# Performance work log

Hardware: AMD Instinct MI355X
Metric: run time of the kernel (lower is better)

## Reference

```python
import jax, jax.numpy as jnp
import numpy as np

D_K = 64  # head dim used for scaling, matches init d_k


def setup_inputs() -> dict:
    key = jax.random.key(0)
    k1, k2, k3 = jax.random.split(key, 3)
    shape = (2, 2048, 16, 64)  # [batch, seq, heads, head_dim]
    q = jax.random.normal(k1, shape, dtype=jnp.float32)
    k = jax.random.normal(k2, shape, dtype=jnp.float32)
    v = jax.random.normal(k3, shape, dtype=jnp.float32)
    return {"q": q, "k": k, "v": v}


def reference(q, k, v):
    # score: [n, h, q, k]
    scale = 1.0 / np.sqrt(D_K).astype(np.float32)
    score = jnp.einsum('nqhd,nkhd->nhqk', q, k) * scale
    attn = jax.nn.softmax(score, axis=-1)
    context = jnp.einsum('nhqk,nkhd->nqhd', attn, v)
    return (context, attn)
```

## Files before the change

kernel.cpp:

```cpp
#include <hip/hip_runtime.h>

#define BATCH 2
#define SEQ   2048
#define NH    16
#define HD    64
#define RS    (NH*HD)
#define NPAIR (BATCH*NH)
#define NKT   (SEQ/64)
#define TILE_SHORTS 4096

typedef float f32x4  __attribute__((ext_vector_type(4)));
typedef short short8 __attribute__((ext_vector_type(8)));

#define GAS __attribute__((address_space(1)))
#define LAS __attribute__((address_space(3)))

__device__ __forceinline__ unsigned f2bf(float f) {
    union { float f; unsigned u; } c; c.f = f;
    return (c.u + 0x7FFFu + ((c.u >> 16) & 1u)) >> 16;
}
__device__ __forceinline__ unsigned pk(float lo, float hi) {
    return f2bf(lo) | (f2bf(hi) << 16);
}
__device__ __forceinline__ int swz(int row, int bc) {
    return (row * 128 + bc) ^ ((row & 7) << 4);
}
__device__ __forceinline__ short8 ld16(const void* p) {
    union { uint4 u; short8 s; } cv;
    cv.u = *(const uint4*)p;
    return cv.s;
}

__device__ __forceinline__ void load_qfrag(const float* Qr, int ks, short8& bq0, short8& bq1) {
    union { unsigned u[4]; short8 s; } t;
    float4 f0 = *(const float4*)(Qr + ks * 8);
    float4 f1 = *(const float4*)(Qr + ks * 8 + 4);
    t.u[0] = pk(f0.x * 0.125f, f0.y * 0.125f);
    t.u[1] = pk(f0.z * 0.125f, f0.w * 0.125f);
    t.u[2] = pk(f1.x * 0.125f, f1.y * 0.125f);
    t.u[3] = pk(f1.z * 0.125f, f1.w * 0.125f);
    bq0 = t.s;
    float4 g0 = *(const float4*)(Qr + 32 + ks * 8);
    float4 g1 = *(const float4*)(Qr + 32 + ks * 8 + 4);
    t.u[0] = pk(g0.x * 0.125f, g0.y * 0.125f);
    t.u[1] = pk(g0.z * 0.125f, g0.w * 0.125f);
    t.u[2] = pk(g1.x * 0.125f, g1.y * 0.125f);
    t.u[3] = pk(g1.z * 0.125f, g1.w * 0.125f);
    bq1 = t.s;
}

__device__ __forceinline__ void stage_k_from_f32(const float* Kt, unsigned short* Ksh, int tid) {
    #pragma unroll
    for (int i = 0; i < 2; ++i) {
        int cidx = tid + i * 256;
        int c = cidx >> 7, j = (cidx >> 6) & 1, l = cidx & 63;
        const float* src = Kt + (c * 16 + (l & 15)) * RS + j * 32 + (l >> 4) * 8;
        float4 f0 = *(const float4*)src;
        float4 f1 = *(const float4*)(src + 4);
        uint4 o = { pk(f0.x, f0.y), pk(f0.z, f0.w), pk(f1.x, f1.y), pk(f1.z, f1.w) };
        *((uint4*)Ksh + cidx) = o;
    }
}

extern "C" __global__ __launch_bounds__(256)
void pack_kv(const float* __restrict__ k, const float* __restrict__ v,
             unsigned short* __restrict__ ktl, unsigned short* __restrict__ vtl)
{
    __shared__ float Vf[64 * 65];
    const int bid = blockIdx.x;
    const int tid = threadIdx.x;

    if (bid < NPAIR * NKT) {
        const int kti = bid & 31, h = (bid >> 5) & 15, n = bid >> 9;
        const float* Kg = k + (((long)n * SEQ + kti * 64) * NH + h) * HD;
        stage_k_from_f32(Kg, ktl + (long)bid * TILE_SHORTS, tid);
    } else {
        const int b2 = bid - NPAIR * NKT;
        const int kti = b2 & 31, h = (b2 >> 5) & 15, n = b2 >> 9;
        const float* Vg = v + (((long)n * SEQ + kti * 64) * NH + h) * HD;
        #pragma unroll
        for (int i = 0; i < 4; ++i) {
            int idx = tid + i * 256;
            int row = idx >> 4, c4 = idx & 15;
            float4 f = *(const float4*)(Vg + row * RS + c4 * 4);
            Vf[row * 65 + c4 * 4 + 0] = f.x;
            Vf[row * 65 + c4 * 4 + 1] = f.y;
            Vf[row * 65 + c4 * 4 + 2] = f.z;
            Vf[row * 65 + c4 * 4 + 3] = f.w;
        }
        __syncthreads();
        uint4* out = (uint4*)(vtl + (long)b2 * TILE_SHORTS);
        #pragma unroll
        for (int i = 0; i < 2; ++i) {
            int cidx = tid + i * 256;
            int c = cidx >> 7, j = (cidx >> 6) & 1, l = cidx & 63;
            int d = c * 16 + (l & 15);
            int kb = j * 32 + (l >> 4) * 8;
            float a0 = Vf[(kb + 0) * 65 + d], a1 = Vf[(kb + 1) * 65 + d];
            float a2 = Vf[(kb + 2) * 65 + d], a3 = Vf[(kb + 3) * 65 + d];
            float a4 = Vf[(kb + 4) * 65 + d], a5 = Vf[(kb + 5) * 65 + d];
            float a6 = Vf[(kb + 6) * 65 + d], a7 = Vf[(kb + 7) * 65 + d];
            uint4 o = { pk(a0, a1), pk(a2, a3), pk(a4, a5), pk(a6, a7) };
            out[cidx] = o;
        }
    }
}

extern "C" __global__ __launch_bounds__(256, 4)
void sdpa_kernel(const float* __restrict__ q,
                 const unsigned short* __restrict__ ktl,
                 const unsigned short* __restrict__ vtl,
                 float* __restrict__ ctx, float* __restrict__ attn,
                 float* __restrict__ linv_out, int skip_pair)
{
    __shared__ unsigned short Kd[2][TILE_SHORTS];
    __shared__ unsigned short Vd[2][TILE_SHORTS];
    __shared__ unsigned short Ps[4][1024];

    const int bid0 = blockIdx.x;
    const int bid  = ((bid0 & 7) << 7) | (bid0 >> 3);
    const int qt = bid & 31, pair = bid >> 5;
    const int h = pair & 15, n = pair >> 4;
    const int tid = threadIdx.x;
    const int w = tid >> 6, lane = tid & 63, lh = lane & 15, ks = lane >> 4;
    const bool wattn = (pair != skip_pair);

    const float* Qr = q + (((long)n * SEQ + qt * 64 + w * 16 + lh) * NH + h) * HD;
    short8 bq0, bq1;
    load_qfrag(Qr, ks, bq0, bq1);

    const unsigned short* Ktile = ktl + (long)pair * NKT * TILE_SHORTS;
    const unsigned short* Vtile = vtl + (long)pair * NKT * TILE_SHORTS;

    auto stage = [&](unsigned short* lbuf, const unsigned short* gt) {
        #pragma unroll
        for (int i = 0; i < 2; ++i) {
            const unsigned short* g = gt + w * 1024 + i * 512 + lane * 8;
            unsigned short* l = lbuf + w * 1024 + i * 512;
            __builtin_amdgcn_global_load_lds((const GAS unsigned int*)g,
                                             (LAS unsigned int*)l, 16, 0, 0);
        }
    };

    stage(Kd[0], Ktile);
    asm volatile("s_waitcnt vmcnt(0)" ::: "memory");
    __builtin_amdgcn_s_barrier();
    float lsum = 0.f;
    for (int kt = 0; kt < NKT; ++kt) {
        const int cur = kt & 1;
        if (kt < NKT - 1) stage(Kd[cur ^ 1], Ktile + (kt + 1) * TILE_SHORTS);
        const char* Kb = (const char*)Kd[cur];
        #pragma unroll
        for (int c = 0; c < 4; ++c) {
            short8 a0 = ld16(Kb + ((c * 2 + 0) * 64 + lane) * 16);
            short8 a1 = ld16(Kb + ((c * 2 + 1) * 64 + lane) * 16);
            f32x4 z = {0.f, 0.f, 0.f, 0.f};
            z = __builtin_amdgcn_mfma_f32_16x16x32_bf16(a0, bq0, z, 0, 0, 0);
            z = __builtin_amdgcn_mfma_f32_16x16x32_bf16(a1, bq1, z, 0, 0, 0);
            lsum += __expf(z[0]) + __expf(z[1]) + __expf(z[2]) + __expf(z[3]);
        }
        asm volatile("s_waitcnt vmcnt(0)" ::: "memory");
        __builtin_amdgcn_s_barrier();
    }
    lsum += __shfl_xor(lsum, 16);
    lsum += __shfl_xor(lsum, 32);
    const float linv = 1.0f / lsum;

    if (pair == skip_pair && linv_out && ks == 0) {
        linv_out[qt * 64 + w * 16 + lh] = linv;
    }

    f32x4 oacc[4];
    #pragma unroll
    for (int cd = 0; cd < 4; ++cd) oacc[cd] = (f32x4){0.f, 0.f, 0.f, 0.f};

    float* attnW = attn + (((long)pair) * SEQ + qt * 64 + w * 16 + lh) * SEQ + ks * 4;
    char* Pw = (char*)Ps[w];

    stage(Kd[0], Ktile);
    stage(Vd[0], Vtile);
    asm volatile("s_waitcnt vmcnt(0)" ::: "memory");
    __builtin_amdgcn_s_barrier();

    for (int kt = 0; kt < NKT; ++kt) {
        const int cur = kt & 1;
        if (kt < NKT - 1) {
            stage(Kd[cur ^ 1], Ktile + (kt + 1) * TILE_SHORTS);
            stage(Vd[cur ^ 1], Vtile + (kt + 1) * TILE_SHORTS);
        }
        asm volatile("" ::: "memory");

        const char* Kb = (const char*)Kd[cur];
        f32x4 s[4];
        #pragma unroll
        for (int c = 0; c < 4; ++c) {
            short8 a0 = ld16(Kb + ((c * 2 + 0) * 64 + lane) * 16);
            short8 a1 = ld16(Kb + ((c * 2 + 1) * 64 + lane) * 16);
            f32x4 z = {0.f, 0.f, 0.f, 0.f};
            z = __builtin_amdgcn_mfma_f32_16x16x32_bf16(a0, bq0, z, 0, 0, 0);
            z = __builtin_amdgcn_mfma_f32_16x16x32_bf16(a1, bq1, z, 0, 0, 0);
            s[c] = z;
        }
        #pragma unroll
        for (int c = 0; c < 4; ++c) {
            f32x4 pv;
            pv[0] = __expf(s[c][0]) * linv;
            pv[1] = __expf(s[c][1]) * linv;
            pv[2] = __expf(s[c][2]) * linv;
            pv[3] = __expf(s[c][3]) * linv;
            if (wattn) {
                __builtin_nontemporal_store(pv, (f32x4*)(attnW + (long)kt * 64 + c * 16));
            }
            uint2 u2 = { pk(pv[0], pv[1]), pk(pv[2], pv[3]) };
            *(uint2*)(Pw + swz(lh, c * 32 + ks * 8)) = u2;
        }
        short8 pa0 = ld16(Pw + swz(lh, ks * 16));
        short8 pa1 = ld16(Pw + swz(lh, 64 + ks * 16));
        const char* Vb = (const char*)Vd[cur];
        #pragma unroll
        for (int cd = 0; cd < 4; ++cd) {
            short8 bv0 = ld16(Vb + ((cd * 2 + 0) * 64 + lane) * 16);
            short8 bv1 = ld16(Vb + ((cd * 2 + 1) * 64 + lane) * 16);
            oacc[cd] = __builtin_amdgcn_mfma_f32_16x16x32_bf16(pa0, bv0, oacc[cd], 0, 0, 0);
            oacc[cd] = __builtin_amdgcn_mfma_f32_16x16x32_bf16(pa1, bv1, oacc[cd], 0, 0, 0);
        }
        if (kt < NKT - 1) {
            if (wattn) asm volatile("s_waitcnt vmcnt(4)" ::: "memory");
            else       asm volatile("s_waitcnt vmcnt(0)" ::: "memory");
            __builtin_amdgcn_s_barrier();
        }
    }

    float* ctxW = ctx + (((long)n * SEQ + qt * 64 + w * 16 + ks * 4) * NH + h) * HD + lh;
    #pragma unroll
    for (int cd = 0; cd < 4; ++cd) {
        #pragma unroll
        for (int r = 0; r < 4; ++r) {
            ctxW[r * RS + cd * 16] = oacc[cd][r];
        }
    }
}

extern "C" __global__ __launch_bounds__(256)
void attn_fill_fast(const float* __restrict__ q, const float* __restrict__ k,
                    float* __restrict__ attn, const float* __restrict__ linv_in,
                    int pair)
{
    __shared__ unsigned short Ksh[TILE_SHORTS];
    const int n = pair >> 4, h = pair & 15;
    const int qt = blockIdx.x & 31, kt = blockIdx.x >> 5;
    const int tid = threadIdx.x;
    const int w = tid >> 6, lane = tid & 63, lh = lane & 15, ks = lane >> 4;

    const float* Qr = q + (((long)n * SEQ + qt * 64 + w * 16 + lh) * NH + h) * HD;
    short8 bq0, bq1;
    load_qfrag(Qr, ks, bq0, bq1);
    const float linv = linv_in[qt * 64 + w * 16 + lh];

    const float* Kt = k + (((long)n * SEQ + kt * 64) * NH + h) * HD;
    stage_k_from_f32(Kt, Ksh, tid);
    __syncthreads();

    float* attnW = attn + (((long)pair) * SEQ + qt * 64 + w * 16 + lh) * SEQ + ks * 4;
    #pragma unroll
    for (int c = 0; c < 4; ++c) {
        short8 a0 = ld16((const char*)Ksh + ((c * 2 + 0) * 64 + lane) * 16);
        short8 a1 = ld16((const char*)Ksh + ((c * 2 + 1) * 64 + lane) * 16);
        f32x4 z = {0.f, 0.f, 0.f, 0.f};
        z = __builtin_amdgcn_mfma_f32_16x16x32_bf16(a0, bq0, z, 0, 0, 0);
        z = __builtin_amdgcn_mfma_f32_16x16x32_bf16(a1, bq1, z, 0, 0, 0);
        f32x4 pv;
        pv[0] = __expf(z[0]) * linv;
        pv[1] = __expf(z[1]) * linv;
        pv[2] = __expf(z[2]) * linv;
        pv[3] = __expf(z[3]) * linv;
        __builtin_nontemporal_store(pv, (f32x4*)(attnW + (long)kt * 64 + c * 16));
    }
}

extern "C" __global__ __launch_bounds__(256, 4)
void attn_fill_slow(const float* __restrict__ q, const float* __restrict__ k,
                    float* __restrict__ attn, int pair)
{
    __shared__ unsigned short Ksh[TILE_SHORTS];
    const int n = pair >> 4, h = pair & 15;
    const int qt = blockIdx.x;
    const int tid = threadIdx.x;
    const int w = tid >> 6, lane = tid & 63, lh = lane & 15, ks = lane >> 4;

    const float* Qr = q + (((long)n * SEQ + qt * 64 + w * 16 + lh) * NH + h) * HD;
    short8 bq0, bq1;
    load_qfrag(Qr, ks, bq0, bq1);

    const float* Kg = k + ((long)n * SEQ * NH + h) * HD;

    float lsum = 0.f;
    for (int kt = 0; kt < NKT; ++kt) {
        __syncthreads();
        stage_k_from_f32(Kg + (long)kt * 64 * RS, Ksh, tid);
        __syncthreads();
        #pragma unroll
        for (int c = 0; c < 4; ++c) {
            short8 a0 = ld16((const char*)Ksh + ((c * 2 + 0) * 64 + lane) * 16);
            short8 a1 = ld16((const char*)Ksh + ((c * 2 + 1) * 64 + lane) * 16);
            f32x4 z = {0.f, 0.f, 0.f, 0.f};
            z = __builtin_amdgcn_mfma_f32_16x16x32_bf16(a0, bq0, z, 0, 0, 0);
            z = __builtin_amdgcn_mfma_f32_16x16x32_bf16(a1, bq1, z, 0, 0, 0);
            lsum += __expf(z[0]) + __expf(z[1]) + __expf(z[2]) + __expf(z[3]);
        }
    }
    lsum += __shfl_xor(lsum, 16);
    lsum += __shfl_xor(lsum, 32);
    const float linv = 1.0f / lsum;

    float* attnW = attn + (((long)pair) * SEQ + qt * 64 + w * 16 + lh) * SEQ + ks * 4;
    for (int kt = 0; kt < NKT; ++kt) {
        __syncthreads();
        stage_k_from_f32(Kg + (long)kt * 64 * RS, Ksh, tid);
        __syncthreads();
        #pragma unroll
        for (int c = 0; c < 4; ++c) {
            short8 a0 = ld16((const char*)Ksh + ((c * 2 + 0) * 64 + lane) * 16);
            short8 a1 = ld16((const char*)Ksh + ((c * 2 + 1) * 64 + lane) * 16);
            f32x4 z = {0.f, 0.f, 0.f, 0.f};
            z = __builtin_amdgcn_mfma_f32_16x16x32_bf16(a0, bq0, z, 0, 0, 0);
            z = __builtin_amdgcn_mfma_f32_16x16x32_bf16(a1, bq1, z, 0, 0, 0);
            f32x4 pv;
            pv[0] = __expf(z[0]) * linv;
            pv[1] = __expf(z[1]) * linv;
            pv[2] = __expf(z[2]) * linv;
            pv[3] = __expf(z[3]) * linv;
            *(f32x4*)(attnW + (long)kt * 64 + c * 16) = pv;
        }
    }
}

extern "C" void kernel_launch(void* const* d_in, const int* in_sizes, int n_in,
                              void* d_out, int out_size, void* d_ws, size_t ws_size,
                              hipStream_t stream)
{
    const float* q = (const float*)d_in[0];
    const float* k = (const float*)d_in[1];
    const float* v = (const float*)d_in[2];
    float* ctx  = (float*)d_out;
    float* attn = ctx + (size_t)BATCH * SEQ * NH * HD;

    const size_t tiles_shorts = (size_t)NPAIR * NKT * TILE_SHORTS;
    const size_t ws_need = 2 * tiles_shorts * sizeof(unsigned short);

    unsigned short *ktl, *vtl;
    int skip;
    if (ws_size >= ws_need) {
        ktl = (unsigned short*)d_ws;
        vtl = ktl + tiles_shorts;
        skip = -1;
    } else {
        ktl = (unsigned short*)(attn + (size_t)(NPAIR - 1) * SEQ * SEQ);
        vtl = ktl + tiles_shorts;
        skip = NPAIR - 1;
    }

    const bool linv_fits = (ws_size >= SEQ * sizeof(float));
    float* linv_ws = (skip >= 0 && linv_fits) ? (float*)d_ws : nullptr;

    hipLaunchKernelGGL(pack_kv, dim3(2 * NPAIR * NKT), dim3(256), 0, stream, k, v, ktl, vtl);
    hipLaunchKernelGGL(sdpa_kernel, dim3(NPAIR * NKT), dim3(256), 0, stream,
                       q, ktl, vtl, ctx, attn, linv_ws, skip);
    if (skip >= 0) {
        if (linv_ws) {
            hipLaunchKernelGGL(attn_fill_fast, dim3(NKT * 32), dim3(256), 0, stream,
                               q, k, attn, linv_ws, skip);
        } else {
            hipLaunchKernelGGL(attn_fill_slow, dim3(32), dim3(256), 0, stream, q, k, attn, skip);
        }
    }
}
```

Baseline: 208.6 us.

## Deepen K prefetch in row-sum pass and fold normalization into exp2

The first pass, which only computes softmax row sums, now prefetches K tiles two steps ahead through a four-buffer ring. It waits on a partial vmcnt with one barrier per step instead of draining all loads each iteration. The second pass computes probabilities as exp2(s*log2e - log2(sum)), replacing exp followed by a multiply. It also uses the hardware packed bf16 convert instead of software rounding and switches attention stores from nontemporal to regular stores. The combined shared-memory buffers are reused across both passes. The store cache-policy change and the different rounding path could shift behaviour or accuracy slightly.

```diff
diff --git a/kernel.cpp b/kernel.cpp
--- a/kernel.cpp
+++ b/kernel.cpp
@@ -113,8 +113,7 @@
                  float* __restrict__ ctx, float* __restrict__ attn,
                  float* __restrict__ linv_out, int skip_pair)
 {
-    __shared__ unsigned short Kd[2][TILE_SHORTS];
-    __shared__ unsigned short Vd[2][TILE_SHORTS];
+    __shared__ unsigned short SM[4][TILE_SHORTS];
     __shared__ unsigned short Ps[4][1024];
 
     const int bid0 = blockIdx.x;
@@ -142,14 +141,20 @@
         }
     };
 
-    stage(Kd[0], Ktile);
-    asm volatile("s_waitcnt vmcnt(0)" ::: "memory");
-    __builtin_amdgcn_s_barrier();
+    stage(SM[0], Ktile);
+    stage(SM[1], Ktile + TILE_SHORTS);
     float lsum = 0.f;
     for (int kt = 0; kt < NKT; ++kt) {
-        const int cur = kt & 1;
-        if (kt < NKT - 1) stage(Kd[cur ^ 1], Ktile + (kt + 1) * TILE_SHORTS);
-        const char* Kb = (const char*)Kd[cur];
+        if (kt + 2 < NKT) {
+            stage(SM[(kt + 2) & 3], Ktile + (long)(kt + 2) * TILE_SHORTS);
+            asm volatile("s_waitcnt vmcnt(4)" ::: "memory");
+        } else if (kt + 1 < NKT) {
+            asm volatile("s_waitcnt vmcnt(2)" ::: "memory");
+        } else {
+            asm volatile("s_waitcnt vmcnt(0)" ::: "memory");
+        }
+        __builtin_amdgcn_s_barrier();
+        const char* Kb = (const char*)SM[kt & 3];
         #pragma unroll
         for (int c = 0; c < 4; ++c) {
             short8 a0 = ld16(Kb + ((c * 2 + 0) * 64 + lane) * 16);
@@ -159,12 +164,11 @@
             z = __builtin_amdgcn_mfma_f32_16x16x32_bf16(a1, bq1, z, 0, 0, 0);
             lsum += __expf(z[0]) + __expf(z[1]) + __expf(z[2]) + __expf(z[3]);
         }
-        asm volatile("s_waitcnt vmcnt(0)" ::: "memory");
-        __builtin_amdgcn_s_barrier();
     }
     lsum += __shfl_xor(lsum, 16);
     lsum += __shfl_xor(lsum, 32);
     const float linv = 1.0f / lsum;
+    const float nml2 = -__log2f(lsum);
 
     if (pair == skip_pair && linv_out && ks == 0) {
         linv_out[qt * 64 + w * 16 + lh] = linv;
@@ -177,20 +181,20 @@
     float* attnW = attn + (((long)pair) * SEQ + qt * 64 + w * 16 + lh) * SEQ + ks * 4;
     char* Pw = (char*)Ps[w];
 
-    stage(Kd[0], Ktile);
-    stage(Vd[0], Vtile);
+    stage(SM[0], Ktile);
+    stage(SM[2], Vtile);
     asm volatile("s_waitcnt vmcnt(0)" ::: "memory");
     __builtin_amdgcn_s_barrier();
 
     for (int kt = 0; kt < NKT; ++kt) {
         const int cur = kt & 1;
         if (kt < NKT - 1) {
-            stage(Kd[cur ^ 1], Ktile + (kt + 1) * TILE_SHORTS);
-            stage(Vd[cur ^ 1], Vtile + (kt + 1) * TILE_SHORTS);
+            stage(SM[cur ^ 1], Ktile + (long)(kt + 1) * TILE_SHORTS);
+            stage(SM[2 + (cur ^ 1)], Vtile + (long)(kt + 1) * TILE_SHORTS);
         }
         asm volatile("" ::: "memory");
 
-        const char* Kb = (const char*)Kd[cur];
+        const char* Kb = (const char*)SM[cur];
         f32x4 s[4];
         #pragma unroll
         for (int c = 0; c < 4; ++c) {
@@ -204,19 +208,19 @@
         #pragma unroll
         for (int c = 0; c < 4; ++c) {
             f32x4 pv;
-            pv[0] = __expf(s[c][0]) * linv;
-            pv[1] = __expf(s[c][1]) * linv;
-            pv[2] = __expf(s[c][2]) * linv;
-            pv[3] = __expf(s[c][3]) * linv;
-            if (wattn) {
-                __builtin_nontemporal_store(pv, (f32x4*)(attnW + (long)kt * 64 + c * 16));
-            }
-            uint2 u2 = { pk(pv[0], pv[1]), pk(pv[2], pv[3]) };
+            #pragma unroll
+            for (int r = 0; r < 4; ++r)
+                pv[r] = __builtin_amdgcn_exp2f(fmaf(s[c][r], 1.44269504f, nml2));
+            if (wattn) *(f32x4*)(attnW + (long)kt * 64 + c * 16) = pv;
+            unsigned r0, r1;
+            asm("v_cvt_pk_bf16_f32 %0, %1, %2" : "=v"(r0) : "v"(pv[0]), "v"(pv[1]));
+            asm("v_cvt_pk_bf16_f32 %0, %1, %2" : "=v"(r1) : "v"(pv[2]), "v"(pv[3]));
+            uint2 u2 = { r0, r1 };
             *(uint2*)(Pw + swz(lh, c * 32 + ks * 8)) = u2;
         }
         short8 pa0 = ld16(Pw + swz(lh, ks * 16));
         short8 pa1 = ld16(Pw + swz(lh, 64 + ks * 16));
-        const char* Vb = (const char*)Vd[cur];
+        const char* Vb = (const char*)SM[2 + cur];
         #pragma unroll
         for (int cd = 0; cd < 4; ++cd) {
             short8 bv0 = ld16(Vb + ((cd * 2 + 0) * 64 + lane) * 16);
@@ -274,7 +278,7 @@
         pv[1] = __expf(z[1]) * linv;
         pv[2] = __expf(z[2]) * linv;
         pv[3] = __expf(z[3]) * linv;
-        __builtin_nontemporal_store(pv, (f32x4*)(attnW + (long)kt * 64 + c * 16));
+        *(f32x4*)(attnW + (long)kt * 64 + c * 16) = pv;
     }
 }
 
```

Measured after the change: 187.7 us. -10.0%, faster.
